# Kernel optimization log

Hardware: AMD Instinct MI355X
Metric: run time of the kernel (lower is better)

## Reference

```python
import jax, jax.numpy as jnp
import numpy as np

B, N, D, S, ITERS = 32, 4096, 256, 7, 3
EPS_LN = 1e-5

def _ln(x, g, b):
    m = jnp.mean(x, axis=-1, keepdims=True)
    v = jnp.mean((x - m) ** 2, axis=-1, keepdims=True)
    return g * (x - m) * jax.lax.rsqrt(v + EPS_LN) + b

def setup_inputs() -> dict:
    key = jax.random.key(0)
    ks = jax.random.split(key, 16)
    w = lambda k, shape: (jax.random.normal(k, shape, jnp.float32) * 0.02)
    return {
        "inputs": jax.random.normal(ks[0], (B, N, D), jnp.float32),
        "noise": jax.random.normal(ks[1], (B, S, D), jnp.float32),
        "ln_in_g": jnp.ones((D,), jnp.float32), "ln_in_b": jnp.zeros((D,), jnp.float32),
        "ln_slots_g": jnp.ones((D,), jnp.float32), "ln_slots_b": jnp.zeros((D,), jnp.float32),
        "ln_mlp_g": jnp.ones((D,), jnp.float32), "ln_mlp_b": jnp.zeros((D,), jnp.float32),
        "slots_mu": w(ks[2], (1, 1, D)),
        "slots_sigma": jnp.ones((1, 1, D), jnp.float32),
        "wq": w(ks[3], (D, D)), "bq": jnp.zeros((D,), jnp.float32),
        "wk": w(ks[4], (D, D)), "bk": jnp.zeros((D,), jnp.float32),
        "wv": w(ks[5], (D, D)), "bv": jnp.zeros((D,), jnp.float32),
        "w_ih": w(ks[6], (3 * D, D)), "b_ih": jnp.zeros((3 * D,), jnp.float32),
        "w_hh": w(ks[7], (3 * D, D)), "b_hh": jnp.zeros((3 * D,), jnp.float32),
        "w1": w(ks[8], (2 * D, D)), "b1": jnp.zeros((2 * D,), jnp.float32),
        "w2": w(ks[9], (D, 2 * D)), "b2": jnp.zeros((D,), jnp.float32),
    }

def reference(inputs, noise, ln_in_g, ln_in_b, ln_slots_g, ln_slots_b, ln_mlp_g, ln_mlp_b,
              slots_mu, slots_sigma, wq, bq, wk, bk, wv, bv,
              w_ih, b_ih, w_hh, b_hh, w1, b1, w2, b2):
    x = _ln(inputs, ln_in_g, ln_in_b)                      # [B,N,D]
    sigma = jax.nn.softplus(slots_sigma)
    slots = slots_mu + sigma * noise                       # [B,S,D]
    k = x @ wk.T + bk                                      # [B,N,D]
    v = x @ wv.T + bv                                      # [B,N,D]
    scale = D ** -0.5
    attn = None
    for _ in range(ITERS):
        slots_prev = slots
        q = _ln(slots, ln_slots_g, ln_slots_b) @ wq.T + bq  # [B,S,D]
        logits = jnp.einsum('bsd,bnd->bsn', q, k) * scale   # [B,S,N]
        attn = jax.nn.softmax(logits, axis=1) + 1e-8        # softmax over slots
        attn = attn / jnp.sum(attn, axis=-1, keepdims=True)
        updates = jnp.einsum('bsn,bnd->bsd', attn, v)       # [B,S,D]
        # GRUCell(updates, slots_prev), torch gate order (r, z, n)
        gi = updates @ w_ih.T + b_ih                        # [B,S,3D]
        gh = slots_prev @ w_hh.T + b_hh
        i_r, i_z, i_n = jnp.split(gi, 3, axis=-1)
        h_r, h_z, h_n = jnp.split(gh, 3, axis=-1)
        r = jax.nn.sigmoid(i_r + h_r)
        z = jax.nn.sigmoid(i_z + h_z)
        n = jnp.tanh(i_n + r * h_n)
        slots = (1.0 - z) * n + z * slots_prev
        h = jax.nn.relu(_ln(slots, ln_mlp_g, ln_mlp_b) @ w1.T + b1)
        slots = slots + h @ w2.T + b2
    return slots, jnp.swapaxes(attn, 1, 2)                 # [B,S,D], [B,N,S]
```

## Files before the change

### kernel.cpp

```cpp
#include <hip/hip_runtime.h>
#include <stdint.h>

typedef unsigned short u16;
typedef unsigned int u32;
typedef float f32x4 __attribute__((ext_vector_type(4)));
typedef short short8 __attribute__((ext_vector_type(8)));

#define NBAT 32
#define NSEQ 4096
#define ND 256
#define NSLOT 7
#define NCHUNK 64

__device__ __forceinline__ u32 bf16rne(float f){
  u32 u = __float_as_uint(f);
  u = u + 0x7FFFu + ((u >> 16) & 1u);
  return u >> 16;
}
__device__ __forceinline__ u32 packbf(float a, float b){
  return (bf16rne(a) & 0xFFFFu) | (bf16rne(b) << 16);
}
__device__ __forceinline__ float bflo(u32 u){ return __uint_as_float(u << 16); }
__device__ __forceinline__ float bfhi(u32 u){ return __uint_as_float(u & 0xFFFF0000u); }

__device__ __forceinline__ void gld16(void* lds, const void* g){
  __builtin_amdgcn_global_load_lds(
      (const __attribute__((address_space(1))) u32*)g,
      (__attribute__((address_space(3))) u32*)lds, 16, 0, 0);
}

__global__ __launch_bounds__(256) void k_prep(
    const float* __restrict__ wk, const float* __restrict__ wv,
    const float* __restrict__ bk, const float* __restrict__ bv,
    const float* __restrict__ mu, const float* __restrict__ sig,
    const float* __restrict__ noise,
    const float* __restrict__ w_ih, const float* __restrict__ b_ih,
    const float* __restrict__ w_hh, const float* __restrict__ b_hh,
    const float* __restrict__ w1, const float* __restrict__ w2,
    const float* __restrict__ wq,
    u16* __restrict__ Wkv, float* __restrict__ biaskv, float* __restrict__ slots,
    u16* __restrict__ Wg, u16* __restrict__ w1b, u16* __restrict__ w2b,
    u16* __restrict__ wqb, float* __restrict__ bg){
  const int bid = blockIdx.x, t = threadIdx.x;
  if (bid < 512){
    const float* src = (bid < 256) ? (wk + (size_t)bid*256) : (wv + (size_t)(bid-256)*256);
    Wkv[(size_t)bid*256 + t] = (u16)bf16rne(src[t]);
  } else if (bid == 512){
    biaskv[t] = bk[t];
    biaskv[256 + t] = bv[t];
  } else if (bid < 737){
    int r = bid - 513;
    float sp = logf(1.f + expf(sig[t]));
    slots[(size_t)r*256 + t] = mu[t] + sp * noise[(size_t)r*256 + t];
  } else if (bid < 1761){
    int j = bid - 737;
    u16 a, b;
    if (j < 512){ a = (u16)bf16rne(w_ih[(size_t)j*256 + t]); b = (u16)bf16rne(w_hh[(size_t)j*256 + t]); }
    else if (j < 768){ a = (u16)bf16rne(w_ih[(size_t)j*256 + t]); b = 0; }
    else { a = 0; b = (u16)bf16rne(w_hh[(size_t)(j-256)*256 + t]); }
    Wg[(size_t)j*512 + t] = a;
    Wg[(size_t)j*512 + 256 + t] = b;
  } else if (bid < 2273){
    int j = bid - 1761;
    w1b[(size_t)j*256 + t] = (u16)bf16rne(w1[(size_t)j*256 + t]);
  } else if (bid < 2529){
    int j = bid - 2273;
    w2b[(size_t)j*512 + t]       = (u16)bf16rne(w2[(size_t)j*512 + t]);
    w2b[(size_t)j*512 + 256 + t] = (u16)bf16rne(w2[(size_t)j*512 + 256 + t]);
  } else if (bid < 2785){
    int j = bid - 2529;
    wqb[(size_t)j*256 + t] = (u16)bf16rne(wq[(size_t)j*256 + t]);
  } else {
#pragma unroll
    for (int ii = 0; ii < 4; ++ii){
      int j = ii*256 + t;
      float v;
      if (j < 512) v = b_ih[j] + b_hh[j];
      else if (j < 768) v = b_ih[j];
      else v = b_hh[j - 256];
      bg[j] = v;
    }
  }
}

__global__ __launch_bounds__(256) void k_ln_in(
    const float* __restrict__ x, const float* __restrict__ g, const float* __restrict__ b,
    u16* __restrict__ xo){
  const int row = blockIdx.x*4 + (threadIdx.x >> 6);
  const int lane = threadIdx.x & 63;
  const f32x4 v = *(const f32x4*)(x + (size_t)row*ND + lane*4);
  float s  = v[0]+v[1]+v[2]+v[3];
  float s2 = v[0]*v[0]+v[1]*v[1]+v[2]*v[2]+v[3]*v[3];
#pragma unroll
  for (int m = 1; m < 64; m <<= 1){ s += __shfl_xor(s, m); s2 += __shfl_xor(s2, m); }
  const float mean = s * (1.f/256.f);
  const float var  = s2 * (1.f/256.f) - mean*mean;
  const float rstd = rsqrtf(var + 1e-5f);
  const f32x4 gg = *(const f32x4*)(g + lane*4);
  const f32x4 bb = *(const f32x4*)(b + lane*4);
  float y0 = (v[0]-mean)*rstd*gg[0] + bb[0];
  float y1 = (v[1]-mean)*rstd*gg[1] + bb[1];
  float y2 = (v[2]-mean)*rstd*gg[2] + bb[2];
  float y3 = (v[3]-mean)*rstd*gg[3] + bb[3];
  uint2 o; o.x = packbf(y0, y1); o.y = packbf(y2, y3);
  *(uint2*)(xo + (size_t)row*ND + lane*4) = o;
}

__global__ __launch_bounds__(256) void k_gemm_kv(
    const u16* __restrict__ X, const u16* __restrict__ W,
    const float* __restrict__ biaskv, u16* __restrict__ kv){
  __shared__ __align__(16) u16 At[2][128*64];
  __shared__ __align__(16) u16 Bt[2][128*64];
  const int bid = blockIdx.x;
  const int swz = ((bid & 7) << 9) + (bid >> 3);
  const int mb = swz >> 2, nb = swz & 3;
  const int tid = threadIdx.x, w = tid >> 6, lane = tid & 63;
  const int wm = w >> 1, wn = w & 1;
  f32x4 acc[4][4];
#pragma unroll
  for (int a = 0; a < 4; ++a)
#pragma unroll
    for (int c = 0; c < 4; ++c) acc[a][c] = (f32x4){0.f,0.f,0.f,0.f};

  const int cl = lane & 7;
#define STAGE_KV(buf, kt)                                                        \
  {                                                                              \
    _Pragma("unroll")                                                            \
    for (int i = 0; i < 4; ++i){                                                 \
      int R = w*32 + i*8 + (lane >> 3);                                          \
      int c = cl ^ (R & 7);                                                      \
      gld16(&At[buf][(w*32 + i*8)*64], X + ((size_t)(mb*128 + R))*256 + (kt)*64 + c*8); \
      gld16(&Bt[buf][(w*32 + i*8)*64], W + ((size_t)(nb*128 + R))*256 + (kt)*64 + c*8); \
    }                                                                            \
  }
  STAGE_KV(0, 0);
  __syncthreads();
  for (int kt = 0; kt < 4; ++kt){
    const int cur = kt & 1;
    if (kt < 3) STAGE_KV(cur ^ 1, kt + 1);
#pragma unroll
    for (int kk = 0; kk < 2; ++kk){
      short8 xf[4], wf[4];
#pragma unroll
      for (int xi = 0; xi < 4; ++xi){
        int r = wm*64 + xi*16 + (lane & 15);
        int ch = (kk*4 + (lane >> 4)) ^ (r & 7);
        xf[xi] = *(const short8*)&At[cur][r*64 + ch*8];
      }
#pragma unroll
      for (int wi = 0; wi < 4; ++wi){
        int r = wn*64 + wi*16 + (lane & 15);
        int ch = (kk*4 + (lane >> 4)) ^ (r & 7);
        wf[wi] = *(const short8*)&Bt[cur][r*64 + ch*8];
      }
#pragma unroll
      for (int xi = 0; xi < 4; ++xi)
#pragma unroll
        for (int wi = 0; wi < 4; ++wi)
          acc[xi][wi] = __builtin_amdgcn_mfma_f32_16x16x32_bf16(wf[wi], xf[xi], acc[xi][wi], 0, 0, 0);
    }
    __syncthreads();
  }
#undef STAGE_KV
  f32x4 bias[4];
#pragma unroll
  for (int wi = 0; wi < 4; ++wi)
    bias[wi] = *(const f32x4*)(biaskv + nb*128 + wn*64 + wi*16 + (lane >> 4)*4);
#pragma unroll
  for (int xi = 0; xi < 4; ++xi){
    size_t m = (size_t)mb*128 + wm*64 + xi*16 + (lane & 15);
    u16* dst = kv + m*512 + nb*128 + wn*64 + (lane >> 4)*4;
#pragma unroll
    for (int wi = 0; wi < 4; ++wi){
      f32x4 c = acc[xi][wi];
      uint2 o;
      o.x = packbf(c[0] + bias[wi][0], c[1] + bias[wi][1]);
      o.y = packbf(c[2] + bias[wi][2], c[3] + bias[wi][3]);
      *(uint2*)(dst + wi*16) = o;
    }
  }
}

template<int MODE>
__global__ __launch_bounds__(256) void k_gemm_s(
    const u16* __restrict__ A, const u16* __restrict__ W,
    const float* __restrict__ bias, int nkt,
    float* __restrict__ outf, u16* __restrict__ outb,
    const float* __restrict__ snew, float* __restrict__ out2, int last){
  __shared__ __align__(16) u16 At[2][128*64];
  __shared__ __align__(16) u16 Bt[2][128*64];
  const int nb = blockIdx.x, mb = blockIdx.y;
  const int tid = threadIdx.x, w = tid >> 6, lane = tid & 63;
  const int wm = w >> 1, wn = w & 1;
  const size_t K = (size_t)nkt * 64;
  f32x4 acc[4][4];
#pragma unroll
  for (int a = 0; a < 4; ++a)
#pragma unroll
    for (int c = 0; c < 4; ++c) acc[a][c] = (f32x4){0.f,0.f,0.f,0.f};

  const int cl = lane & 7;
#define STAGE_S(buf, kt)                                                         \
  {                                                                              \
    _Pragma("unroll")                                                            \
    for (int i = 0; i < 4; ++i){                                                 \
      int R = w*32 + i*8 + (lane >> 3);                                          \
      int c = cl ^ (R & 7);                                                      \
      gld16(&At[buf][(w*32 + i*8)*64], A + ((size_t)(mb*128 + R))*K + (kt)*64 + c*8); \
      gld16(&Bt[buf][(w*32 + i*8)*64], W + ((size_t)(nb*128 + R))*K + (kt)*64 + c*8); \
    }                                                                            \
  }
  STAGE_S(0, 0);
  __syncthreads();
  for (int kt = 0; kt < nkt; ++kt){
    const int cur = kt & 1;
    if (kt < nkt - 1) STAGE_S(cur ^ 1, kt + 1);
#pragma unroll
    for (int kk = 0; kk < 2; ++kk){
      short8 xf[4], wf[4];
#pragma unroll
      for (int xi = 0; xi < 4; ++xi){
        int r = wm*64 + xi*16 + (lane & 15);
        int ch = (kk*4 + (lane >> 4)) ^ (r & 7);
        xf[xi] = *(const short8*)&At[cur][r*64 + ch*8];
      }
#pragma unroll
      for (int wi = 0; wi < 4; ++wi){
        int r = wn*64 + wi*16 + (lane & 15);
        int ch = (kk*4 + (lane >> 4)) ^ (r & 7);
        wf[wi] = *(const short8*)&Bt[cur][r*64 + ch*8];
      }
#pragma unroll
      for (int xi = 0; xi < 4; ++xi)
#pragma unroll
        for (int wi = 0; wi < 4; ++wi)
          acc[xi][wi] = __builtin_amdgcn_mfma_f32_16x16x32_bf16(wf[wi], xf[xi], acc[xi][wi], 0, 0, 0);
    }
    __syncthreads();
  }
#undef STAGE_S
  const int LDO = (MODE == 0) ? 1024 : ((MODE == 1) ? 512 : 256);
  f32x4 b4[4];
#pragma unroll
  for (int wi = 0; wi < 4; ++wi)
    b4[wi] = *(const f32x4*)(bias + nb*128 + wn*64 + wi*16 + (lane >> 4)*4);
#pragma unroll
  for (int xi = 0; xi < 4; ++xi){
    const int m = mb*128 + wm*64 + xi*16 + (lane & 15);
    const int colb = nb*128 + wn*64 + (lane >> 4)*4;
#pragma unroll
    for (int wi = 0; wi < 4; ++wi){
      const int col = colb + wi*16;
      f32x4 c = acc[xi][wi] + b4[wi];
      if (MODE == 0){
        *(f32x4*)(outf + (size_t)m*LDO + col) = c;
      } else if (MODE == 1){
        uint2 o;
        o.x = packbf(fmaxf(c[0],0.f), fmaxf(c[1],0.f));
        o.y = packbf(fmaxf(c[2],0.f), fmaxf(c[3],0.f));
        *(uint2*)(outb + (size_t)m*LDO + col) = o;
      } else if (MODE == 2){
        if (m < 224){
          const f32x4 s4 = *(const f32x4*)(snew + (size_t)m*256 + col);
          f32x4 o = c + s4;
          *(f32x4*)(outf + (size_t)m*LDO + col) = o;
          if (last) *(f32x4*)(out2 + (size_t)m*LDO + col) = o;
        }
      } else {
        uint2 o;
        o.x = packbf(c[0]*0.09016844f, c[1]*0.09016844f);
        o.y = packbf(c[2]*0.09016844f, c[3]*0.09016844f);
        *(uint2*)(outb + (size_t)m*LDO + col) = o;
      }
    }
  }
}

__global__ __launch_bounds__(256) void k_attn(
    const u16* __restrict__ kv, const u16* __restrict__ qb,
    float* __restrict__ attn_out, float* __restrict__ pacc, float* __restrict__ pw){
  __shared__ __align__(16) float accbuf[4][7][256];
  __shared__ __align__(16) float p_lds[4][16][8];
  __shared__ float wsum_lds[4][8];
  const int chunk = blockIdx.x, b = blockIdx.y;
  const int tid = threadIdx.x, w = tid >> 6, lane = tid & 63;
  const int l15 = lane & 15, g = lane >> 4, hi = lane >> 5;
  const size_t bbase = (size_t)b*NSEQ;
  const int nr0 = chunk*64 + w*16;

  short8 qf[8];
  {
    const u16* qrow = qb + ((size_t)b*7 + l15)*256;
#pragma unroll
    for (int ks = 0; ks < 8; ++ks)
      qf[ks] = *(const short8*)(qrow + (ks*4 + g)*8);
  }
  f32x4 z = {0.f,0.f,0.f,0.f};
#pragma unroll
  for (int ks = 0; ks < 8; ++ks){
    const short8 kf = *(const short8*)(kv + (bbase + nr0 + l15)*512 + (ks*4 + g)*8);
    z = __builtin_amdgcn_mfma_f32_16x16x32_bf16(qf[ks], kf, z, 0, 0, 0);
  }
  float zz[4];
#pragma unroll
  for (int j = 0; j < 4; ++j){
    const int s = g*4 + j;
    zz[j] = (s < 7) ? z[j] : -3.0e38f;
  }
  float mx = fmaxf(fmaxf(zz[0], zz[1]), fmaxf(zz[2], zz[3]));
  mx = fmaxf(mx, __shfl_xor(mx, 16));
  float p[4], psum = 0.f;
#pragma unroll
  for (int j = 0; j < 4; ++j){ p[j] = exp2f(zz[j] - mx); psum += p[j]; }
  psum += __shfl_xor(psum, 16);
  const float rs = 1.f / psum;
#pragma unroll
  for (int j = 0; j < 4; ++j) p[j] = fmaf(p[j], rs, 1e-8f);
  float wloc[4] = {0.f,0.f,0.f,0.f};
  if (lane < 32){
    *(f32x4*)&p_lds[w][l15][g*4] = (f32x4){p[0], p[1], p[2], p[3]};
    const size_t arow = (bbase + nr0 + l15)*7;
#pragma unroll
    for (int j = 0; j < 4; ++j){
      const int s = g*4 + j;
      if (s < 7){ attn_out[arow + s] = p[j]; wloc[j] = p[j]; }
    }
  }
  __syncthreads();
  float acc[7][4];
#pragma unroll
  for (int s = 0; s < 7; ++s){ acc[s][0]=acc[s][1]=acc[s][2]=acc[s][3]=0.f; }
#pragma unroll
  for (int it = 0; it < 8; ++it){
    const int rm = it*2 + hi, ro = it*2 + (1 - hi);
    const uint2 va = *(const uint2*)(kv + (bbase + nr0 + rm)*512 + 256 + (size_t)lane*4);
    const uint2 vb = *(const uint2*)(kv + (bbase + nr0 + ro)*512 + 256 + (size_t)lane*4);
    const f32x4 pm0 = *(const f32x4*)&p_lds[w][rm][0];
    const f32x4 pm1 = *(const f32x4*)&p_lds[w][rm][4];
    const f32x4 po0 = *(const f32x4*)&p_lds[w][ro][0];
    const f32x4 po1 = *(const f32x4*)&p_lds[w][ro][4];
    const float pm[7] = {pm0[0],pm0[1],pm0[2],pm0[3],pm1[0],pm1[1],pm1[2]};
    const float po[7] = {po0[0],po0[1],po0[2],po0[3],po1[0],po1[1],po1[2]};
    const float vm0=bflo(va.x), vm1=bfhi(va.x), vm2=bflo(va.y), vm3=bfhi(va.y);
    const float vo0=bflo(vb.x), vo1=bfhi(vb.x), vo2=bflo(vb.y), vo3=bfhi(vb.y);
#pragma unroll
    for (int s = 0; s < 7; ++s){
      acc[s][0] = fmaf(pm[s], vm0, fmaf(po[s], vo0, acc[s][0]));
      acc[s][1] = fmaf(pm[s], vm1, fmaf(po[s], vo1, acc[s][1]));
      acc[s][2] = fmaf(pm[s], vm2, fmaf(po[s], vo2, acc[s][2]));
      acc[s][3] = fmaf(pm[s], vm3, fmaf(po[s], vo3, acc[s][3]));
    }
  }
#pragma unroll
  for (int m = 1; m < 16; m <<= 1){
#pragma unroll
    for (int j = 0; j < 4; ++j) wloc[j] += __shfl_xor(wloc[j], m);
  }
  if (lane < 32 && l15 == 0){
#pragma unroll
    for (int j = 0; j < 4; ++j) wsum_lds[w][g*4 + j] = wloc[j];
  }
  __syncthreads();
#pragma unroll
  for (int s = 0; s < 7; ++s)
    *(f32x4*)&accbuf[w][s][lane*4] = (f32x4){acc[s][0], acc[s][1], acc[s][2], acc[s][3]};
  __syncthreads();
#pragma unroll
  for (int s = 0; s < 7; ++s){
    float sum = accbuf[0][s][tid] + accbuf[1][s][tid] + accbuf[2][s][tid] + accbuf[3][s][tid];
    pacc[((size_t)chunk*NBAT + b)*(NSLOT*256) + s*256 + tid] = sum;
  }
  if (tid < 7)
    pw[((size_t)chunk*NBAT + b)*NSLOT + tid] =
        wsum_lds[0][tid] + wsum_lds[1][tid] + wsum_lds[2][tid] + wsum_lds[3][tid];
}

__global__ __launch_bounds__(256) void k_slotA(
    const float* __restrict__ pacc, const float* __restrict__ pw,
    const float* __restrict__ slots, u16* __restrict__ A2, float* __restrict__ wsum){
  __shared__ float pwb[NCHUNK];
  const int r = blockIdx.x, t = threadIdx.x;
  if (r >= 224){
    A2[(size_t)r*512 + t] = 0;
    A2[(size_t)r*512 + 256 + t] = 0;
    return;
  }
  if (t < NCHUNK) pwb[t] = pw[(size_t)t*224 + r];
  float u = 0.f;
#pragma unroll 8
  for (int c = 0; c < NCHUNK; ++c) u += pacc[(size_t)c*57344 + (size_t)r*256 + t];
  __syncthreads();
  float wst = 0.f;
#pragma unroll
  for (int c = 0; c < NCHUNK; ++c) wst += pwb[c];
  if (t == 0) wsum[r] = wst;
  A2[(size_t)r*512 + t] = (u16)bf16rne(u / wst);
  A2[(size_t)r*512 + 256 + t] = (u16)bf16rne(slots[(size_t)r*256 + t]);
}

__global__ __launch_bounds__(256) void k_slotB(
    const float* __restrict__ gates, const float* __restrict__ slots,
    const float* __restrict__ gm, const float* __restrict__ bm,
    float* __restrict__ snew, u16* __restrict__ lnm){
  __shared__ float red[8];
  const int r = blockIdx.x, t = threadIdx.x;
  if (r >= 224){ lnm[(size_t)r*256 + t] = 0; return; }
  const float g0  = gates[(size_t)r*1024 + t];
  const float g1  = gates[(size_t)r*1024 + 256 + t];
  const float gin = gates[(size_t)r*1024 + 512 + t];
  const float ghn = gates[(size_t)r*1024 + 768 + t];
  const float spv = slots[(size_t)r*256 + t];
  const float rr = 1.f/(1.f + __expf(-g0));
  const float zz = 1.f/(1.f + __expf(-g1));
  float xx = gin + rr*ghn;
  xx = fminf(fmaxf(xx, -15.f), 15.f);
  const float e2 = __expf(2.f*xx);
  const float nn = (e2 - 1.f)/(e2 + 1.f);
  const float sp = (1.f - zz)*nn + zz*spv;
  snew[(size_t)r*256 + t] = sp;
  float s = sp, s2 = sp*sp;
#pragma unroll
  for (int m = 1; m < 64; m <<= 1){ s += __shfl_xor(s, m); s2 += __shfl_xor(s2, m); }
  if ((t & 63) == 0){ red[t >> 6] = s; red[4 + (t >> 6)] = s2; }
  __syncthreads();
  const float ssum = red[0]+red[1]+red[2]+red[3];
  const float qsum = red[4]+red[5]+red[6]+red[7];
  const float mean = ssum*(1.f/256.f);
  const float var  = qsum*(1.f/256.f) - mean*mean;
  const float rstd = rsqrtf(var + 1e-5f);
  lnm[(size_t)r*256 + t] = (u16)bf16rne((sp - mean)*rstd*gm[t] + bm[t]);
}

__global__ __launch_bounds__(256) void k_lnq(
    const float* __restrict__ slots, const float* __restrict__ g, const float* __restrict__ b,
    u16* __restrict__ lnq){
  __shared__ float red[8];
  const int r = blockIdx.x, t = threadIdx.x;
  if (r >= 224){ lnq[(size_t)r*256 + t] = 0; return; }
  const float x = slots[(size_t)r*256 + t];
  float s = x, s2 = x*x;
#pragma unroll
  for (int m = 1; m < 64; m <<= 1){ s += __shfl_xor(s, m); s2 += __shfl_xor(s2, m); }
  if ((t & 63) == 0){ red[t >> 6] = s; red[4 + (t >> 6)] = s2; }
  __syncthreads();
  const float ssum = red[0]+red[1]+red[2]+red[3];
  const float qsum = red[4]+red[5]+red[6]+red[7];
  const float mean = ssum*(1.f/256.f);
  const float var  = qsum*(1.f/256.f) - mean*mean;
  const float rstd = rsqrtf(var + 1e-5f);
  lnq[(size_t)r*256 + t] = (u16)bf16rne((x - mean)*rstd*g[t] + b[t]);
}

__global__ __launch_bounds__(256) void k_norm(
    float* __restrict__ attn, const float* __restrict__ wsum_tot){
  size_t i = (size_t)blockIdx.x*256 + threadIdx.x;
  int s = (int)(i % 7);
  int b = (int)(i / (NSEQ*7));
  attn[i] = attn[i] / wsum_tot[b*7 + s];
}

extern "C" void kernel_launch(void* const* d_in, const int* in_sizes, int n_in,
                              void* d_out, int out_size, void* d_ws, size_t ws_size,
                              hipStream_t stream){
  (void)in_sizes; (void)n_in; (void)out_size; (void)ws_size;
  const float* inputs  = (const float*)d_in[0];
  const float* noise   = (const float*)d_in[1];
  const float* ln_in_g = (const float*)d_in[2];
  const float* ln_in_b = (const float*)d_in[3];
  const float* ln_sl_g = (const float*)d_in[4];
  const float* ln_sl_b = (const float*)d_in[5];
  const float* ln_ml_g = (const float*)d_in[6];
  const float* ln_ml_b = (const float*)d_in[7];
  const float* mu      = (const float*)d_in[8];
  const float* sig     = (const float*)d_in[9];
  const float* wq      = (const float*)d_in[10];
  const float* bq      = (const float*)d_in[11];
  const float* wk      = (const float*)d_in[12];
  const float* bk      = (const float*)d_in[13];
  const float* wv      = (const float*)d_in[14];
  const float* bv      = (const float*)d_in[15];
  const float* w_ih    = (const float*)d_in[16];
  const float* b_ih    = (const float*)d_in[17];
  const float* w_hh    = (const float*)d_in[18];
  const float* b_hh    = (const float*)d_in[19];
  const float* w1      = (const float*)d_in[20];
  const float* b1      = (const float*)d_in[21];
  const float* w2      = (const float*)d_in[22];
  const float* b2      = (const float*)d_in[23];

  char* ws = (char*)d_ws;
  u16*   x_bf   = (u16*)(ws);
  u16*   kv     = (u16*)(ws + 67108864);
  char*  paccch = ws + 201326592;
  float* pacc   = (float*)paccch;
  u16*   Wkv    = (u16*)(ws + 216006656);
  u16*   qeffb  = (u16*)(ws + 216268800);
  float* slots  = (float*)(ws + 216530944);
  float* pw     = (float*)(ws + 216760320);
  float* biaskv = (float*)(ws + 216817664);
  float* wsum   = (float*)(ws + 216819712);
  u16*   A2     = (u16*)(ws + 216820736);
  u16*   Wg     = (u16*)(ws + 217082880);
  u16*   w1b    = (u16*)(ws + 218131456);
  u16*   w2b    = (u16*)(ws + 218393600);
  u16*   wqb    = (u16*)(ws + 218655744);
  float* bg     = (float*)(ws + 218786816);

  float* gates  = (float*)(paccch);
  u16*   hb     = (u16*)(paccch + 1048576);
  u16*   lnm    = (u16*)(paccch + 1310720);
  u16*   lnq    = (u16*)(paccch + 1441792);
  float* snew   = (float*)(paccch + 1572864);

  float* out_slots = (float*)d_out;
  float* attn = (float*)d_out + 57344;

  k_prep<<<2786, 256, 0, stream>>>(wk, wv, bk, bv, mu, sig, noise,
                                   w_ih, b_ih, w_hh, b_hh, w1, w2, wq,
                                   Wkv, biaskv, slots, Wg, w1b, w2b, wqb, bg);
  k_ln_in<<<32768, 256, 0, stream>>>(inputs, ln_in_g, ln_in_b, x_bf);
  k_gemm_kv<<<4096, 256, 0, stream>>>(x_bf, Wkv, biaskv, kv);
  for (int i = 0; i < 3; ++i){
    const int last = (i == 2) ? 1 : 0;
    k_lnq<<<256, 256, 0, stream>>>(slots, ln_sl_g, ln_sl_b, lnq);
    k_gemm_s<3><<<dim3(2, 2), 256, 0, stream>>>(lnq, wqb, bq, 4, nullptr, qeffb, nullptr, nullptr, 0);
    k_attn<<<dim3(NCHUNK, 32), 256, 0, stream>>>(kv, qeffb, attn, pacc, pw);
    k_slotA<<<256, 256, 0, stream>>>(pacc, pw, slots, A2, wsum);
    k_gemm_s<0><<<dim3(8, 2), 256, 0, stream>>>(A2, Wg, bg, 8, gates, nullptr, nullptr, nullptr, 0);
    k_slotB<<<256, 256, 0, stream>>>(gates, slots, ln_ml_g, ln_ml_b, snew, lnm);
    k_gemm_s<1><<<dim3(4, 2), 256, 0, stream>>>(lnm, w1b, b1, 4, nullptr, hb, nullptr, nullptr, 0);
    k_gemm_s<2><<<dim3(2, 2), 256, 0, stream>>>(hb, w2b, b2, 8, slots, nullptr, snew, out_slots, last);
  }
  k_norm<<<3584, 256, 0, stream>>>(attn, wsum);
}
```

Before: 373.3 us.

## Load K/V weight fragments directly from global and single-buffer the activation tile

The K/V projection GEMM no longer stages the weight tile through LDS. Each wave reads its weight MFMA fragments straight from global memory (L2-resident) into registers, and the activation tile is single-buffered in shared memory with two barriers per k-step. This cuts LDS use from 64KB to 16KB per block, which may allow more blocks per CU and removes LDS traffic for the weights. In exchange it gives up double-buffered prefetch overlap and adds uncoalesced global fragment loads.

```diff
diff --git a/kernel.cpp b/kernel.cpp
--- a/kernel.cpp
+++ b/kernel.cpp
@@ -109,13 +109,13 @@
 __global__ __launch_bounds__(256) void k_gemm_kv(
     const u16* __restrict__ X, const u16* __restrict__ W,
     const float* __restrict__ biaskv, u16* __restrict__ kv){
-  __shared__ __align__(16) u16 At[2][128*64];
-  __shared__ __align__(16) u16 Bt[2][128*64];
+  __shared__ __align__(16) u16 At[128*64];
   const int bid = blockIdx.x;
   const int swz = ((bid & 7) << 9) + (bid >> 3);
   const int mb = swz >> 2, nb = swz & 3;
   const int tid = threadIdx.x, w = tid >> 6, lane = tid & 63;
   const int wm = w >> 1, wn = w & 1;
+  const int l15 = lane & 15, g = lane >> 4;
   f32x4 acc[4][4];
 #pragma unroll
   for (int a = 0; a < 4; ++a)
@@ -123,53 +123,46 @@
     for (int c = 0; c < 4; ++c) acc[a][c] = (f32x4){0.f,0.f,0.f,0.f};
 
   const int cl = lane & 7;
-#define STAGE_KV(buf, kt)                                                        \
-  {                                                                              \
-    _Pragma("unroll")                                                            \
-    for (int i = 0; i < 4; ++i){                                                 \
-      int R = w*32 + i*8 + (lane >> 3);                                          \
-      int c = cl ^ (R & 7);                                                      \
-      gld16(&At[buf][(w*32 + i*8)*64], X + ((size_t)(mb*128 + R))*256 + (kt)*64 + c*8); \
-      gld16(&Bt[buf][(w*32 + i*8)*64], W + ((size_t)(nb*128 + R))*256 + (kt)*64 + c*8); \
-    }                                                                            \
-  }
-  STAGE_KV(0, 0);
-  __syncthreads();
+  const u16* wbase = W + ((size_t)(nb*128 + wn*64 + l15))*256;
   for (int kt = 0; kt < 4; ++kt){
-    const int cur = kt & 1;
-    if (kt < 3) STAGE_KV(cur ^ 1, kt + 1);
+    short8 wf[2][4];
+#pragma unroll
+    for (int kk = 0; kk < 2; ++kk)
+#pragma unroll
+      for (int wi = 0; wi < 4; ++wi)
+        wf[kk][wi] = *(const short8*)(wbase + (size_t)wi*16*256 + kt*64 + (kk*4 + g)*8);
+    __syncthreads();
+#pragma unroll
+    for (int i = 0; i < 4; ++i){
+      int R = w*32 + i*8 + (lane >> 3);
+      int c = cl ^ (R & 7);
+      gld16(&At[(w*32 + i*8)*64], X + ((size_t)(mb*128 + R))*256 + kt*64 + c*8);
+    }
+    __syncthreads();
 #pragma unroll
     for (int kk = 0; kk < 2; ++kk){
-      short8 xf[4], wf[4];
+      short8 xf[4];
 #pragma unroll
       for (int xi = 0; xi < 4; ++xi){
-        int r = wm*64 + xi*16 + (lane & 15);
-        int ch = (kk*4 + (lane >> 4)) ^ (r & 7);
-        xf[xi] = *(const short8*)&At[cur][r*64 + ch*8];
+        int r = wm*64 + xi*16 + l15;
+        int ch = (kk*4 + g) ^ (r & 7);
+        xf[xi] = *(const short8*)&At[r*64 + ch*8];
       }
 #pragma unroll
-      for (int wi = 0; wi < 4; ++wi){
-        int r = wn*64 + wi*16 + (lane & 15);
-        int ch = (kk*4 + (lane >> 4)) ^ (r & 7);
-        wf[wi] = *(const short8*)&Bt[cur][r*64 + ch*8];
-      }
-#pragma unroll
       for (int xi = 0; xi < 4; ++xi)
 #pragma unroll
         for (int wi = 0; wi < 4; ++wi)
-          acc[xi][wi] = __builtin_amdgcn_mfma_f32_16x16x32_bf16(wf[wi], xf[xi], acc[xi][wi], 0, 0, 0);
-    }
-    __syncthreads();
-  }
-#undef STAGE_KV
+          acc[xi][wi] = __builtin_amdgcn_mfma_f32_16x16x32_bf16(wf[kk][wi], xf[xi], acc[xi][wi], 0, 0, 0);
+    }
+  }
   f32x4 bias[4];
 #pragma unroll
   for (int wi = 0; wi < 4; ++wi)
-    bias[wi] = *(const f32x4*)(biaskv + nb*128 + wn*64 + wi*16 + (lane >> 4)*4);
+    bias[wi] = *(const f32x4*)(biaskv + nb*128 + wn*64 + wi*16 + g*4);
 #pragma unroll
   for (int xi = 0; xi < 4; ++xi){
-    size_t m = (size_t)mb*128 + wm*64 + xi*16 + (lane & 15);
-    u16* dst = kv + m*512 + nb*128 + wn*64 + (lane >> 4)*4;
+    size_t m = (size_t)mb*128 + wm*64 + xi*16 + l15;
+    u16* dst = kv + m*512 + nb*128 + wn*64 + g*4;
 #pragma unroll
     for (int wi = 0; wi < 4; ++wi){
       f32x4 c = acc[xi][wi];
```

New measurement: 397.9 us. 1.07x slower.
